# Kernel tuning notes

Measured on AMD Instinct MI355X. Metric: run time of the kernel, lower is better.

Reference implementation:

```python
import jax, jax.numpy as jnp
import numpy as np

B, T, C, K = 8, 4096, 256, 4  # batch, time, d_embd, k_periods


def setup_inputs() -> dict:
    key = jax.random.key(0)
    ks = jax.random.split(key, 5)
    x = jax.random.normal(ks[0], (B, T, C), jnp.float32)
    # inception stand-in: masked 3x3 conv (HWIO) + GELU
    Wc = jax.random.normal(ks[1], (3, 3, C, C), jnp.float32) * 0.02
    bc = jnp.zeros((C,), jnp.float32)
    # FeedForward params
    W1 = jax.random.normal(ks[2], (C, 4 * C), jnp.float32) * 0.02
    b1 = jnp.zeros((4 * C,), jnp.float32)
    W2 = jax.random.normal(ks[3], (4 * C, C), jnp.float32) * 0.02
    b2 = jnp.zeros((C,), jnp.float32)
    return {"x": x, "Wc": Wc, "bc": bc, "W1": W1, "b1": b1, "W2": W2, "b2": b2}


def _topk_freq_idx(x):
    # eager (concrete) period detection; shapes downstream are data-dependent,
    # exactly like the torch original (which is also not compilable as one graph)
    xf = jnp.fft.rfft(x, axis=1)[:, 1:, :]            # drop DC -> [B, T//2, C]
    amps_full = jnp.mean(jnp.abs(xf), axis=-1)        # [B, T//2]
    _, idx = jax.lax.top_k(amps_full, K)              # [B, K] indices into sliced bins
    return np.asarray(jax.device_get(idx))


def _fold(x, n):
    # vectorized per-sample 1D->2D folding with period n[b]; returns masked grid
    pad = (T - T % n) % n
    m = (T + pad) // n
    M, N = int(m.max()), int(n.max())
    nj = jnp.asarray(n)[:, None, None]                # [B,1,1]
    i = jnp.arange(M)[None, :, None]
    j = jnp.arange(N)[None, None, :]
    t = i * nj + j                                    # [B,M,N] flat time index
    valid = (j < nj) & (t < T)
    tc = jnp.clip(t, 0, T - 1)
    grid = x[jnp.arange(B)[:, None, None], tc] * valid[..., None]  # [B,M,N,C]
    mask = valid[..., None].astype(x.dtype)
    return grid, mask


def _inception(grid, mask, Wc, bc):
    y = jax.lax.conv_general_dilated(
        grid, Wc, window_strides=(1, 1), padding='SAME',
        dimension_numbers=('NHWC', 'HWIO', 'NHWC'))
    return jax.nn.gelu(y + bc, approximate=False) * mask


def _unfold(y, n):
    ts = jnp.arange(T)[None, :]
    nj = jnp.asarray(n)[:, None]
    return y[jnp.arange(B)[:, None], ts // nj, ts % nj]  # [B,T,C]


def _forward(x, Wc, bc, W1, b1, W2, b2, idx_np):
    # differentiable amplitude recomputation with fixed (closed-over) indices
    xf = jnp.fft.rfft(x, axis=1)[:, 1:, :]
    amps_full = jnp.mean(jnp.abs(xf), axis=-1)                     # [B, T//2]
    amps_k = jnp.take_along_axis(amps_full, jnp.asarray(idx_np), axis=1)  # [B,K]
    # original computes p = T // topk_index; clamp to avoid div-by-zero on idx 0
    p = np.maximum(T // np.maximum(idx_np, 1), 1)                   # [B,K] np ints
    outs = []
    for k in range(K):
        grid, mask = _fold(x, p[:, k])
        y = _inception(grid, mask, Wc, bc)
        outs.append(_unfold(y, p[:, k]))
    tf = jnp.stack(outs, axis=1)                                   # [B,K,T,C]
    h = jax.nn.gelu(tf @ W1 + b1, approximate=False) @ W2 + b2     # FeedForward
    w = jax.nn.softmax(amps_k, axis=-1)[:, :, None, None]
    return x + (h * w).sum(axis=1)


def reference(x, Wc, bc, W1, b1, W2, b2):
    idx_np = _topk_freq_idx(x)
    return _forward(x, Wc, bc, W1, b1, W2, b2, idx_np)
```

## Files before the change

### kernel.cpp

```cpp
#include <hip/hip_runtime.h>
#include <cstdint>
#include <cstddef>

#define T_LEN 4096
#define C_DIM 256
#define B_DIM 8
#define K_TOP 4

typedef __attribute__((ext_vector_type(8))) short bf16x8;
typedef __attribute__((ext_vector_type(4))) float f32x4;

__device__ __forceinline__ float gelu_fast(float x) {
    float x2 = x * x;
    float a = x * fmaf(0.071354816f, x2, 1.595769122f);
    float e = __expf(-a);
    return __fdividef(x, 1.0f + e);
}

__device__ __forceinline__ unsigned short f2bf(float f) {
    uint32_t u = __float_as_uint(f);
    uint32_t r = (u + 0x7fffu + ((u >> 16) & 1u)) >> 16;
    return (unsigned short)r;
}

typedef __attribute__((address_space(3))) uint32_t lds_u32_t;
typedef __attribute__((address_space(1))) const uint32_t gbl_u32_t;

__device__ __forceinline__ void lds_load16(const void* g, void* l) {
    __builtin_amdgcn_global_load_lds((gbl_u32_t*)g, (lds_u32_t*)l, 16, 0, 0);
}

#define BAR_VM0()                                                      \
    do {                                                               \
        asm volatile("s_waitcnt vmcnt(0) lgkmcnt(0)" ::: "memory");    \
        __builtin_amdgcn_s_barrier();                                  \
        __builtin_amdgcn_sched_barrier(0);                             \
    } while (0)
#define BAR_VM3()                                                      \
    do {                                                               \
        asm volatile("s_waitcnt vmcnt(3) lgkmcnt(0)" ::: "memory");    \
        __builtin_amdgcn_s_barrier();                                  \
        __builtin_amdgcn_sched_barrier(0);                             \
    } while (0)
#define BAR_LGKM()                                                     \
    do {                                                               \
        asm volatile("s_waitcnt lgkmcnt(0)" ::: "memory");             \
        __builtin_amdgcn_s_barrier();                                  \
        __builtin_amdgcn_sched_barrier(0);                             \
    } while (0)

#define FPAD(i) ((i) + ((i) >> 5))

__global__ __launch_bounds__(256) void cvt_x_kernel(const float4* __restrict__ x,
                                                    ushort4* __restrict__ xbf,
                                                    unsigned short* __restrict__ zbuf) {
    size_t i = (size_t)blockIdx.x * 256 + threadIdx.x;
    float4 v = x[i];
    ushort4 o;
    o.x = f2bf(v.x); o.y = f2bf(v.y); o.z = f2bf(v.z); o.w = f2bf(v.w);
    xbf[i] = o;
    if (blockIdx.x == 0 && threadIdx.x < 256) zbuf[threadIdx.x] = 0;
}

__global__ __launch_bounds__(256) void transpose_cvt_kernel(const float* __restrict__ src,
                                                            unsigned short* __restrict__ dst,
                                                            int R, int C) {
    __shared__ float t[32][33];
    const int c0 = blockIdx.x * 32, r0 = blockIdx.y * 32;
    const int lx = threadIdx.x & 31, ly = threadIdx.x >> 5;
    for (int rr = ly; rr < 32; rr += 8) {
        int r = r0 + rr, c = c0 + lx;
        t[rr][lx] = (r < R && c < C) ? src[(size_t)r * C + c] : 0.0f;
    }
    __syncthreads();
    for (int rr = ly; rr < 32; rr += 8) {
        int c = c0 + rr, r = r0 + lx;
        if (r < R && c < C) dst[(size_t)c * R + r] = f2bf(t[lx][rr]);
    }
}

__global__ __launch_bounds__(256) void repack_frag_kernel(const float* __restrict__ src,
                                                          unsigned short* __restrict__ dst,
                                                          int K, int N) {
    int idx = blockIdx.x * 256 + threadIdx.x;
    int total = (N >> 4) * (K >> 5) * 64;
    if (idx >= total) return;
    int lane = idx & 63, tile = idx >> 6;
    int ktiles = K >> 5;
    int tile_n = tile / ktiles, tile_k = tile % ktiles;
    int col = tile_n * 16 + (lane & 15);
    int k0 = tile_k * 32 + (lane >> 4) * 8;
    __align__(16) unsigned short v[8];
#pragma unroll
    for (int j = 0; j < 8; j++) v[j] = f2bf(src[(size_t)(k0 + j) * N + col]);
    *(uint4*)(dst + (size_t)idx * 8) = *(const uint4*)v;
}

__global__ __launch_bounds__(256) void transpose_x_kernel(const float* __restrict__ x,
                                                          float* __restrict__ xT) {
    __shared__ float tile[32][33];
    const int b = blockIdx.z;
    const int t0 = blockIdx.x * 32, c0 = blockIdx.y * 32;
    const int lx = threadIdx.x & 31, ly = threadIdx.x >> 5;
    const float* xp = x + (size_t)b * T_LEN * C_DIM;
    float* op = xT + (size_t)b * C_DIM * T_LEN;
    for (int rr = ly; rr < 32; rr += 8)
        tile[rr][lx] = xp[(size_t)(t0 + rr) * C_DIM + c0 + lx];
    __syncthreads();
    for (int rr = ly; rr < 32; rr += 8)
        op[(size_t)(c0 + rr) * T_LEN + t0 + lx] = tile[lx][rr];
}

__global__ __launch_bounds__(256) void fft_mag_kernel(const float* __restrict__ src,
                                                      float* __restrict__ mags,
                                                      int transposed) {
    const int bx = blockIdx.x;
    const int b = bx >> 8;
    const int c = bx & 255;
    const int tid = threadIdx.x;

    __shared__ __align__(16) float re[4224];
    __shared__ __align__(16) float im[4224];
    __shared__ __align__(16) float twr[2048];
    __shared__ __align__(16) float twi[2048];

    for (int u = tid; u < 2048; u += 256) {
        float ang = -6.283185307179586f * (float)u / 4096.0f;
        float s, co;
        sincosf(ang, &s, &co);
        twr[u] = co;
        twi[u] = s;
    }
    for (int i = tid; i < 4224; i += 256) im[i] = 0.0f;

    if (transposed) {
        const float4* row = (const float4*)(src + ((size_t)(b * C_DIM + c)) * T_LEN);
        for (int e4 = tid; e4 < 1024; e4 += 256) {
            float4 v = row[e4];
            int e = e4 * 4;
            re[FPAD((int)(__brev((unsigned)(e + 0)) >> 20))] = v.x;
            re[FPAD((int)(__brev((unsigned)(e + 1)) >> 20))] = v.y;
            re[FPAD((int)(__brev((unsigned)(e + 2)) >> 20))] = v.z;
            re[FPAD((int)(__brev((unsigned)(e + 3)) >> 20))] = v.w;
        }
    } else {
        const float* xp = src + (size_t)b * T_LEN * C_DIM + c;
        for (int e = tid; e < 4096; e += 256) {
            int r = (int)(__brev((unsigned)e) >> 20);
            re[FPAD(r)] = xp[(size_t)e * C_DIM];
        }
    }
    __syncthreads();

#pragma unroll
    for (int sp = 0; sp < 6; sp++) {
        const int h = 1 << (2 * sp);
        const int t1s = 11 - 2 * sp;
        const int t2s = 10 - 2 * sp;
        for (int j = tid; j < 1024; j += 256) {
            int p = j & (h - 1);
            int G = j >> (2 * sp);
            int base = G * 4 * h + p;
            int iA = FPAD(base), iB = FPAD(base + h);
            int iC = FPAD(base + 2 * h), iD = FPAD(base + 3 * h);
            float w1r = twr[p << t1s], w1i = twi[p << t1s];
            float w2r = twr[p << t2s], w2i = twi[p << t2s];
            float Ar = re[iA], Ai = im[iA], Br = re[iB], Bi = im[iB];
            float Cr = re[iC], Ci = im[iC], Dr = re[iD], Di = im[iD];
            float tBr = w1r * Br - w1i * Bi, tBi = w1r * Bi + w1i * Br;
            float tDr = w1r * Dr - w1i * Di, tDi = w1r * Di + w1i * Dr;
            float A1r = Ar + tBr, A1i = Ai + tBi;
            float B1r = Ar - tBr, B1i = Ai - tBi;
            float C1r = Cr + tDr, C1i = Ci + tDi;
            float D1r = Cr - tDr, D1i = Ci - tDi;
            float tCr = w2r * C1r - w2i * C1i, tCi = w2r * C1i + w2i * C1r;
            float uDr = w2r * D1r - w2i * D1i, uDi = w2r * D1i + w2i * D1r;
            float vDr = uDi, vDi = -uDr;
            re[iA] = A1r + tCr; im[iA] = A1i + tCi;
            re[iC] = A1r - tCr; im[iC] = A1i - tCi;
            re[iB] = B1r + vDr; im[iB] = B1i + vDi;
            re[iD] = B1r - vDr; im[iD] = B1i - vDi;
        }
        __syncthreads();
    }

    float* mp = mags + ((size_t)(b * C_DIM + c)) * 2048;
    for (int u = tid; u < 2048; u += 256) {
        int f = FPAD(u + 1);
        mp[u] = sqrtf(re[f] * re[f] + im[f] * im[f]);
    }
}

__global__ __launch_bounds__(256) void reduce_amps_kernel(const float* __restrict__ mags,
                                                          float* __restrict__ partial) {
    const int b = blockIdx.z, cc = blockIdx.y;
    const int u = blockIdx.x * 256 + threadIdx.x;
    const float* mp = mags + ((size_t)b * C_DIM + cc * 32) * 2048 + u;
    float s = 0.0f;
    for (int c = 0; c < 32; c++) s += mp[(size_t)c * 2048];
    partial[((size_t)b * 8 + cc) * 2048 + u] = s;
}

__global__ __launch_bounds__(256) void topk_kernel(const float* __restrict__ partial,
                                                   int* __restrict__ meta_p,
                                                   float* __restrict__ meta_w) {
    const int b = blockIdx.x;
    const int tid = threadIdx.x;
    __shared__ float v[2048];
    __shared__ float rv[256];
    __shared__ int ri[256];
    __shared__ float topv[K_TOP];
    __shared__ int topi[K_TOP];

    for (int u = tid; u < 2048; u += 256) {
        float s = 0.0f;
        for (int cc = 0; cc < 8; cc++) s += partial[((size_t)b * 8 + cc) * 2048 + u];
        v[u] = s * (1.0f / (float)C_DIM);
    }

    for (int k = 0; k < K_TOP; k++) {
        __syncthreads();
        float bv = -1e30f;
        int bi = 2048;
        for (int u = tid; u < 2048; u += 256) {
            float val = v[u];
            if (val > bv) { bv = val; bi = u; }
        }
        rv[tid] = bv;
        ri[tid] = bi;
        __syncthreads();
        for (int s = 128; s > 0; s >>= 1) {
            if (tid < s) {
                float ov = rv[tid + s];
                int oi = ri[tid + s];
                if (ov > rv[tid] || (ov == rv[tid] && oi < ri[tid])) {
                    rv[tid] = ov;
                    ri[tid] = oi;
                }
            }
            __syncthreads();
        }
        if (tid == 0) {
            topv[k] = rv[0];
            topi[k] = ri[0];
            v[ri[0]] = -1e30f;
        }
    }
    __syncthreads();
    if (tid == 0) {
        float mx = topv[0];
        for (int k = 1; k < K_TOP; k++) mx = fmaxf(mx, topv[k]);
        float e[K_TOP], se = 0.0f;
        for (int k = 0; k < K_TOP; k++) { e[k] = expf(topv[k] - mx); se += e[k]; }
        for (int k = 0; k < K_TOP; k++) {
            int idx = topi[k];
            int d = (idx >= 1) ? idx : 1;
            int p = T_LEN / d;
            if (p < 1) p = 1;
            meta_p[b * K_TOP + k] = p;
            meta_w[b * K_TOP + k] = e[k] / se;
        }
    }
}

__global__ __launch_bounds__(512) void conv_mfma_kernel(const unsigned short* __restrict__ xbf,
                                                        const unsigned short* __restrict__ WcT,
                                                        const float* __restrict__ bc,
                                                        const int* __restrict__ meta_p,
                                                        const unsigned short* __restrict__ zbuf,
                                                        unsigned short* __restrict__ convbufs,
                                                        size_t conv_stride, int koff) {
    const int b = blockIdx.y;
    const int kz = blockIdx.z;
    const int n = meta_p[b * K_TOP + koff + kz];
    const int row0 = blockIdx.x * 128;
    const int tid = threadIdx.x, w = tid >> 6, lane = tid & 63;
    const int wm = w >> 2, wn = w & 3;

    __shared__ __align__(16) unsigned short Al[3][128 * 32];
    __shared__ __align__(16) unsigned short Bl[3][256 * 32];

    const int ra = tid >> 2;
    const int swz = ((tid & 3) ^ ((ra >> 1) & 3)) * 8;
    int ti, tj;
    {
        int t = row0 + ra;
        ti = t / n;
        tj = t - ti * n;
    }
    const unsigned short* xb = xbf + (size_t)b * T_LEN * C_DIM;
    const unsigned short* baseB0 = WcT + (size_t)ra * 2304 + swz;
    const unsigned short* baseB1 = WcT + (size_t)(ra + 128) * 2304 + swz;

    auto computeA = [&](int q) -> const unsigned short* {
        int di = q / 3 - 1, dj = q % 3 - 1;
        int ii = ti + di, jj = tj + dj;
        int tp = ii * n + jj;
        bool ok = (jj >= 0) && (jj < n) && (ii >= 0) && (tp < T_LEN);
        return ok ? (xb + (size_t)tp * C_DIM + swz) : (zbuf + swz);
    };

    f32x4 acc[4][4];
#pragma unroll
    for (int m = 0; m < 4; m++)
#pragma unroll
        for (int nn = 0; nn < 4; nn++) acc[m][nn] = (f32x4){0.f, 0.f, 0.f, 0.f};

    const unsigned short* baseA = computeA(0);
    lds_load16(baseA, &Al[0][tid * 8]);
    lds_load16(baseB0, &Bl[0][tid * 8]);
    lds_load16(baseB1, &Bl[0][4096 + tid * 8]);
    lds_load16(baseA + 32, &Al[1][tid * 8]);
    lds_load16(baseB0 + 32, &Bl[1][tid * 8]);
    lds_load16(baseB1 + 32, &Bl[1][4096 + tid * 8]);

    int cur = 0, stb = 2;
    for (int s = 0; s < 72; s++) {
        if (s < 71) BAR_VM3();
        else        BAR_VM0();

        const int t = s + 2;
        if (t < 72) {
            if ((t & 7) == 0) baseA = computeA(t >> 3);
            lds_load16(baseA + (t & 7) * 32, &Al[stb][tid * 8]);
            lds_load16(baseB0 + (size_t)t * 32, &Bl[stb][tid * 8]);
            lds_load16(baseB1 + (size_t)t * 32, &Bl[stb][4096 + tid * 8]);
        }

        bf16x8 af[4], bfr[4];
#pragma unroll
        for (int m = 0; m < 4; m++) {
            int row = wm * 64 + m * 16 + (lane & 15);
            af[m] = *(const bf16x8*)((const char*)&Al[cur][0] + row * 64 +
                                     (((lane >> 4) * 16) ^ (((row >> 1) & 3) << 4)));
        }
#pragma unroll
        for (int nn = 0; nn < 4; nn++) {
            int rowb = wn * 64 + nn * 16 + (lane & 15);
            bfr[nn] = *(const bf16x8*)((const char*)&Bl[cur][0] + rowb * 64 +
                                       (((lane >> 4) * 16) ^ (((rowb >> 1) & 3) << 4)));
        }
        __builtin_amdgcn_s_setprio(1);
#pragma unroll
        for (int m = 0; m < 4; m++)
#pragma unroll
            for (int nn = 0; nn < 4; nn++)
                acc[m][nn] = __builtin_amdgcn_mfma_f32_16x16x32_bf16(af[m], bfr[nn], acc[m][nn], 0, 0, 0);
        __builtin_amdgcn_s_setprio(0);

        cur = (cur == 2) ? 0 : cur + 1;
        stb = (stb == 2) ? 0 : stb + 1;
    }

    unsigned short* ob = convbufs + (size_t)kz * conv_stride + (size_t)b * T_LEN * C_DIM;
#pragma unroll
    for (int nn = 0; nn < 4; nn++) {
        int col = wn * 64 + nn * 16 + (lane & 15);
        float bs = bc[col];
#pragma unroll
        for (int m = 0; m < 4; m++) {
            int rbase = row0 + wm * 64 + m * 16 + (lane >> 4) * 4;
#pragma unroll
            for (int r = 0; r < 4; r++) {
                float v = acc[m][nn][r] + bs;
                ob[(size_t)(rbase + r) * C_DIM + col] = f2bf(gelu_fast(v));
            }
        }
    }
}

template <int KCNT>
__global__ __launch_bounds__(256, 2) void fused_ff_kernel(
    const unsigned short* __restrict__ convbufs, size_t conv_stride,
    const unsigned short* __restrict__ W1frag,
    const unsigned short* __restrict__ W2frag,
    const float* __restrict__ b1,
    const float* __restrict__ b2,
    const float* __restrict__ meta_w,
    float* __restrict__ out,
    const float* __restrict__ osrc,
    float b2scale, int koff) {
    const int tid = threadIdx.x;
    const int wn = tid >> 6, lane = tid & 63;
    const int row0 = blockIdx.x * 32;
    const int b = row0 >> 12;

    __shared__ __align__(16) unsigned short Asw[KCNT * 32 * 256];
    __shared__ __align__(16) unsigned short Hsw[2][32 * 128];

    float wkv[KCNT];
#pragma unroll
    for (int kc = 0; kc < KCNT; kc++) wkv[kc] = meta_w[b * K_TOP + koff + kc];

    {
        const unsigned short* base = convbufs + (size_t)row0 * C_DIM;
#pragma unroll
        for (int u = 0; u < KCNT * 4; u++) {
            int ch = u * 256 + tid;
            int rfull = ch >> 5;
            int kc = rfull >> 5;
            int trow = rfull & 31;
            int cole = ((ch & 31) * 8) ^ ((rfull & 7) << 3);
            lds_load16(base + (size_t)kc * conv_stride + (size_t)trow * 256 + cole,
                       (unsigned short*)Asw + (size_t)ch * 8);
        }
    }

    f32x4 acc2[2][4];
#pragma unroll
    for (int t2 = 0; t2 < 2; t2++)
#pragma unroll
        for (int nn = 0; nn < 4; nn++) acc2[t2][nn] = (f32x4){0.f, 0.f, 0.f, 0.f};

    BAR_VM0();

    for (int cc = 0; cc < 8; cc++) {
        const int par = cc & 1;

        f32x4 acc1[KCNT][2][2];
#pragma unroll
        for (int kc = 0; kc < KCNT; kc++)
#pragma unroll
            for (int n2 = 0; n2 < 2; n2++)
#pragma unroll
                for (int t2 = 0; t2 < 2; t2++) acc1[kc][n2][t2] = (f32x4){0.f, 0.f, 0.f, 0.f};

        __builtin_amdgcn_s_setprio(1);
#pragma unroll
        for (int ks = 0; ks < 8; ks++) {
            bf16x8 w1f[2];
#pragma unroll
            for (int n2 = 0; n2 < 2; n2++) {
                int tile_n = cc * 8 + wn * 2 + n2;
                w1f[n2] = *(const bf16x8*)(W1frag + ((size_t)(tile_n * 8 + ks) * 64 + lane) * 8);
            }
            bf16x8 af[KCNT][2];
#pragma unroll
            for (int kc = 0; kc < KCNT; kc++)
#pragma unroll
                for (int t2 = 0; t2 < 2; t2++) {
                    int row = kc * 32 + t2 * 16 + (lane & 15);
                    af[kc][t2] = *(const bf16x8*)((const char*)Asw + row * 512 +
                                                  ((ks * 64 + (lane >> 4) * 16) ^ ((row & 7) << 4)));
                }
#pragma unroll
            for (int kc = 0; kc < KCNT; kc++)
#pragma unroll
                for (int n2 = 0; n2 < 2; n2++)
#pragma unroll
                    for (int t2 = 0; t2 < 2; t2++)
                        acc1[kc][n2][t2] = __builtin_amdgcn_mfma_f32_16x16x32_bf16(
                            w1f[n2], af[kc][t2], acc1[kc][n2][t2], 0, 0, 0);
        }
        __builtin_amdgcn_s_setprio(0);

#pragma unroll
        for (int n2 = 0; n2 < 2; n2++) {
            const int hloc = wn * 32 + n2 * 16 + (lane >> 4) * 4;
            f32x4 bb = *(const f32x4*)(b1 + cc * 128 + hloc);
#pragma unroll
            for (int t2 = 0; t2 < 2; t2++) {
                float hc[4];
#pragma unroll
                for (int r = 0; r < 4; r++) {
                    float s = 0.0f;
#pragma unroll
                    for (int kc = 0; kc < KCNT; kc++)
                        s += wkv[kc] * gelu_fast(acc1[kc][n2][t2][r] + bb[r]);
                    hc[r] = s;
                }
                uint32_t lo, hi;
                asm("v_cvt_pk_bf16_f32 %0, %1, %2" : "=v"(lo) : "v"(hc[0]), "v"(hc[1]));
                asm("v_cvt_pk_bf16_f32 %0, %1, %2" : "=v"(hi) : "v"(hc[2]), "v"(hc[3]));
                uint2 pk;
                pk.x = lo;
                pk.y = hi;
                int t = t2 * 16 + (lane & 15);
                *(uint2*)((char*)&Hsw[par][0] + t * 256 +
                          ((hloc * 2) ^ ((t & 7) << 4))) = pk;
            }
        }
        BAR_LGKM();

        __builtin_amdgcn_s_setprio(1);
#pragma unroll
        for (int ks2 = 0; ks2 < 4; ks2++) {
            bf16x8 af2[2], w2f[4];
#pragma unroll
            for (int t2 = 0; t2 < 2; t2++) {
                int row = t2 * 16 + (lane & 15);
                af2[t2] = *(const bf16x8*)((const char*)&Hsw[par][0] + row * 256 +
                                           ((ks2 * 64 + (lane >> 4) * 16) ^ ((row & 7) << 4)));
            }
#pragma unroll
            for (int nn = 0; nn < 4; nn++) {
                int tile_n = wn * 4 + nn;
                int tile_k = cc * 4 + ks2;
                w2f[nn] = *(const bf16x8*)(W2frag + ((size_t)(tile_n * 32 + tile_k) * 64 + lane) * 8);
            }
#pragma unroll
            for (int t2 = 0; t2 < 2; t2++)
#pragma unroll
                for (int nn = 0; nn < 4; nn++)
                    acc2[t2][nn] = __builtin_amdgcn_mfma_f32_16x16x32_bf16(af2[t2], w2f[nn],
                                                                           acc2[t2][nn], 0, 0, 0);
        }
        __builtin_amdgcn_s_setprio(0);
    }

#pragma unroll
    for (int nn = 0; nn < 4; nn++) {
        int col = wn * 64 + nn * 16 + (lane & 15);
        float bb = b2scale * b2[col];
#pragma unroll
        for (int t2 = 0; t2 < 2; t2++) {
            int rbase = row0 + t2 * 16 + (lane >> 4) * 4;
#pragma unroll
            for (int r = 0; r < 4; r++) {
                size_t idx = (size_t)(rbase + r) * C_DIM + col;
                out[idx] = osrc[idx] + acc2[t2][nn][r] + bb;
            }
        }
    }
}

extern "C" void kernel_launch(void* const* d_in, const int* in_sizes, int n_in,
                              void* d_out, int out_size, void* d_ws, size_t ws_size,
                              hipStream_t stream) {
    const float* x  = (const float*)d_in[0];
    const float* Wc = (const float*)d_in[1];
    const float* bc = (const float*)d_in[2];
    const float* W1 = (const float*)d_in[3];
    const float* b1 = (const float*)d_in[4];
    const float* W2 = (const float*)d_in[5];
    const float* b2 = (const float*)d_in[6];
    float* out = (float*)d_out;

    const size_t CONV_ELEMS = (size_t)B_DIM * T_LEN * C_DIM;
    const size_t CONV_BYTES = CONV_ELEMS * 2;
    const size_t MAGS_BYTES = (size_t)B_DIM * C_DIM * 2048 * 4;
    const size_t XT_BYTES = (size_t)B_DIM * T_LEN * C_DIM * 4;

    uint8_t* ws = (uint8_t*)d_ws;
    size_t off = 0;
    auto alloc = [&](size_t bytes) {
        size_t o = off;
        off = (off + bytes + 255) & ~(size_t)255;
        return o;
    };
    float* partial = (float*)(ws + alloc((size_t)B_DIM * 8 * 2048 * 4));
    int* meta_p = (int*)(ws + alloc(B_DIM * K_TOP * 4));
    float* meta_w = (float*)(ws + alloc(B_DIM * K_TOP * 4));
    unsigned short* xbf = (unsigned short*)(ws + alloc((size_t)B_DIM * T_LEN * C_DIM * 2));
    unsigned short* WcT = (unsigned short*)(ws + alloc((size_t)256 * 2304 * 2));
    unsigned short* W1frag = (unsigned short*)(ws + alloc((size_t)256 * 1024 * 2));
    unsigned short* W2frag = (unsigned short*)(ws + alloc((size_t)1024 * 256 * 2));
    unsigned short* zbuf = (unsigned short*)(ws + alloc(512));

    size_t remaining = (ws_size > off) ? (ws_size - off) : 0;
    uint8_t* regionA = ws + off;
    int tier;
    if (remaining >= 4 * CONV_BYTES) tier = 2;
    else if (remaining >= MAGS_BYTES + XT_BYTES) tier = 1;
    else tier = 0;

    float* mags = (float*)regionA;
    float* xT = (float*)(regionA + ((tier == 2) ? CONV_BYTES : MAGS_BYTES));
    unsigned short* convbufs = (unsigned short*)regionA;
    const int use_xT = (tier >= 1);

    cvt_x_kernel<<<dim3((B_DIM * T_LEN * C_DIM / 4) / 256), 256, 0, stream>>>(
        (const float4*)x, (ushort4*)xbf, zbuf);

    transpose_cvt_kernel<<<dim3(256 / 32, 2304 / 32), 256, 0, stream>>>(Wc, WcT, 2304, 256);
    repack_frag_kernel<<<dim3(128), 256, 0, stream>>>(W1, W1frag, 256, 1024);
    repack_frag_kernel<<<dim3(128), 256, 0, stream>>>(W2, W2frag, 1024, 256);

    if (use_xT) {
        transpose_x_kernel<<<dim3(T_LEN / 32, C_DIM / 32, B_DIM), 256, 0, stream>>>(x, xT);
        fft_mag_kernel<<<dim3(B_DIM * C_DIM), 256, 0, stream>>>(xT, mags, 1);
    } else {
        fft_mag_kernel<<<dim3(B_DIM * C_DIM), 256, 0, stream>>>(x, mags, 0);
    }
    reduce_amps_kernel<<<dim3(2048 / 256, 8, B_DIM), 256, 0, stream>>>(mags, partial);
    topk_kernel<<<dim3(B_DIM), 256, 0, stream>>>(partial, meta_p, meta_w);

    if (tier == 2) {
        conv_mfma_kernel<<<dim3(32, B_DIM, K_TOP), 512, 0, stream>>>(
            xbf, WcT, bc, meta_p, zbuf, convbufs, CONV_ELEMS, 0);
        fused_ff_kernel<4><<<dim3(B_DIM * T_LEN / 32), 256, 0, stream>>>(
            convbufs, CONV_ELEMS, W1frag, W2frag, b1, b2, meta_w, out, x, 1.0f, 0);
    } else {
        for (int k = 0; k < K_TOP; k++) {
            conv_mfma_kernel<<<dim3(32, B_DIM, 1), 512, 0, stream>>>(
                xbf, WcT, bc, meta_p, zbuf, convbufs, 0, k);
            fused_ff_kernel<1><<<dim3(B_DIM * T_LEN / 32), 256, 0, stream>>>(
                convbufs, 0, W1frag, W2frag, b1, b2, meta_w, out,
                (k == 0) ? x : out, (k == K_TOP - 1) ? 1.0f : 0.0f, k);
        }
    }
}
```

Baseline: 392.0 us.

## Fuse x bf16 conversion into transpose and store FFT magnitudes as bf16

```diff
diff --git a/kernel.cpp b/kernel.cpp
--- a/kernel.cpp
+++ b/kernel.cpp
@@ -21,6 +21,11 @@
     uint32_t u = __float_as_uint(f);
     uint32_t r = (u + 0x7fffu + ((u >> 16) & 1u)) >> 16;
     return (unsigned short)r;
+}
+
+__device__ __forceinline__ float bf2f(unsigned short v) {
+    uint32_t u = ((uint32_t)v) << 16;
+    return __uint_as_float(u);
 }
 
 typedef __attribute__((address_space(3))) uint32_t lds_u32_t;
@@ -62,6 +67,29 @@
     if (blockIdx.x == 0 && threadIdx.x < 256) zbuf[threadIdx.x] = 0;
 }
 
+__global__ __launch_bounds__(256) void transpose_cvtx_kernel(const float* __restrict__ x,
+                                                             float* __restrict__ xT,
+                                                             unsigned short* __restrict__ xbf,
+                                                             unsigned short* __restrict__ zbuf) {
+    __shared__ float tile[32][33];
+    const int b = blockIdx.z;
+    const int t0 = blockIdx.x * 32, c0 = blockIdx.y * 32;
+    const int lx = threadIdx.x & 31, ly = threadIdx.x >> 5;
+    const float* xp = x + (size_t)b * T_LEN * C_DIM;
+    unsigned short* xbp = xbf + (size_t)b * T_LEN * C_DIM;
+    float* op = xT + (size_t)b * C_DIM * T_LEN;
+    for (int rr = ly; rr < 32; rr += 8) {
+        float v = xp[(size_t)(t0 + rr) * C_DIM + c0 + lx];
+        tile[rr][lx] = v;
+        xbp[(size_t)(t0 + rr) * C_DIM + c0 + lx] = f2bf(v);
+    }
+    __syncthreads();
+    for (int rr = ly; rr < 32; rr += 8)
+        op[(size_t)(c0 + rr) * T_LEN + t0 + lx] = tile[lx][rr];
+    if (blockIdx.x == 0 && blockIdx.y == 0 && blockIdx.z == 0)
+        zbuf[threadIdx.x] = 0;
+}
+
 __global__ __launch_bounds__(256) void transpose_cvt_kernel(const float* __restrict__ src,
                                                             unsigned short* __restrict__ dst,
                                                             int R, int C) {
@@ -96,23 +124,8 @@
     *(uint4*)(dst + (size_t)idx * 8) = *(const uint4*)v;
 }
 
-__global__ __launch_bounds__(256) void transpose_x_kernel(const float* __restrict__ x,
-                                                          float* __restrict__ xT) {
-    __shared__ float tile[32][33];
-    const int b = blockIdx.z;
-    const int t0 = blockIdx.x * 32, c0 = blockIdx.y * 32;
-    const int lx = threadIdx.x & 31, ly = threadIdx.x >> 5;
-    const float* xp = x + (size_t)b * T_LEN * C_DIM;
-    float* op = xT + (size_t)b * C_DIM * T_LEN;
-    for (int rr = ly; rr < 32; rr += 8)
-        tile[rr][lx] = xp[(size_t)(t0 + rr) * C_DIM + c0 + lx];
-    __syncthreads();
-    for (int rr = ly; rr < 32; rr += 8)
-        op[(size_t)(c0 + rr) * T_LEN + t0 + lx] = tile[lx][rr];
-}
-
 __global__ __launch_bounds__(256) void fft_mag_kernel(const float* __restrict__ src,
-                                                      float* __restrict__ mags,
+                                                      unsigned short* __restrict__ mags,
                                                       int transposed) {
     const int bx = blockIdx.x;
     const int b = bx >> 8;
@@ -184,20 +197,20 @@
         __syncthreads();
     }
 
-    float* mp = mags + ((size_t)(b * C_DIM + c)) * 2048;
+    unsigned short* mp = mags + ((size_t)(b * C_DIM + c)) * 2048;
     for (int u = tid; u < 2048; u += 256) {
         int f = FPAD(u + 1);
-        mp[u] = sqrtf(re[f] * re[f] + im[f] * im[f]);
-    }
-}
-
-__global__ __launch_bounds__(256) void reduce_amps_kernel(const float* __restrict__ mags,
+        mp[u] = f2bf(sqrtf(re[f] * re[f] + im[f] * im[f]));
+    }
+}
+
+__global__ __launch_bounds__(256) void reduce_amps_kernel(const unsigned short* __restrict__ mags,
                                                           float* __restrict__ partial) {
     const int b = blockIdx.z, cc = blockIdx.y;
     const int u = blockIdx.x * 256 + threadIdx.x;
-    const float* mp = mags + ((size_t)b * C_DIM + cc * 32) * 2048 + u;
+    const unsigned short* mp = mags + ((size_t)b * C_DIM + cc * 32) * 2048 + u;
     float s = 0.0f;
-    for (int c = 0; c < 32; c++) s += mp[(size_t)c * 2048];
+    for (int c = 0; c < 32; c++) s += bf2f(mp[(size_t)c * 2048]);
     partial[((size_t)b * 8 + cc) * 2048 + u] = s;
 }
 
@@ -538,7 +551,7 @@
 
     const size_t CONV_ELEMS = (size_t)B_DIM * T_LEN * C_DIM;
     const size_t CONV_BYTES = CONV_ELEMS * 2;
-    const size_t MAGS_BYTES = (size_t)B_DIM * C_DIM * 2048 * 4;
+    const size_t MAGS_BYTES = (size_t)B_DIM * C_DIM * 2048 * 2;
     const size_t XT_BYTES = (size_t)B_DIM * T_LEN * C_DIM * 4;
 
     uint8_t* ws = (uint8_t*)d_ws;
@@ -564,20 +577,24 @@
     else if (remaining >= MAGS_BYTES + XT_BYTES) tier = 1;
     else tier = 0;
 
-    float* mags = (float*)regionA;
+    unsigned short* mags = (unsigned short*)regionA;
     float* xT = (float*)(regionA + ((tier == 2) ? CONV_BYTES : MAGS_BYTES));
     unsigned short* convbufs = (unsigned short*)regionA;
     const int use_xT = (tier >= 1);
 
-    cvt_x_kernel<<<dim3((B_DIM * T_LEN * C_DIM / 4) / 256), 256, 0, stream>>>(
-        (const float4*)x, (ushort4*)xbf, zbuf);
+    if (use_xT) {
+        transpose_cvtx_kernel<<<dim3(T_LEN / 32, C_DIM / 32, B_DIM), 256, 0, stream>>>(
+            x, xT, xbf, zbuf);
+    } else {
+        cvt_x_kernel<<<dim3((B_DIM * T_LEN * C_DIM / 4) / 256), 256, 0, stream>>>(
+            (const float4*)x, (ushort4*)xbf, zbuf);
+    }
 
     transpose_cvt_kernel<<<dim3(256 / 32, 2304 / 32), 256, 0, stream>>>(Wc, WcT, 2304, 256);
     repack_frag_kernel<<<dim3(128), 256, 0, stream>>>(W1, W1frag, 256, 1024);
     repack_frag_kernel<<<dim3(128), 256, 0, stream>>>(W2, W2frag, 1024, 256);
 
     if (use_xT) {
-        transpose_x_kernel<<<dim3(T_LEN / 32, C_DIM / 32, B_DIM), 256, 0, stream>>>(x, xT);
         fft_mag_kernel<<<dim3(B_DIM * C_DIM), 256, 0, stream>>>(xT, mags, 1);
     } else {
         fft_mag_kernel<<<dim3(B_DIM * C_DIM), 256, 0, stream>>>(x, mags, 0);
```

New measurement: 385.1 us (median of 2 runs). Within noise of the previous version (-1.8%).
